# Optimization experiments

Measured on AMD Instinct MI355X. Metric: run time of the kernel, lower is better.

## Reference

```python
import jax, jax.numpy as jnp
import numpy as np

B = 4096
IN = 1024
H = 1024
S = 64   # num_memory_slots
Q = 16   # num_qubits_per_slot
OUT = 1024


def setup_inputs() -> dict:
    key = jax.random.key(0)
    ks = jax.random.split(key, 14)
    sd = lambda fan_in: 1.0 / np.sqrt(fan_in)
    return {
        "x_t": jax.random.normal(ks[0], (B, IN), jnp.float32),
        "h_prev": jax.random.normal(ks[1], (B, H), jnp.float32),
        # input_layer: Linear(IN+H, H)
        "W_in": jax.random.normal(ks[2], (IN + H, H), jnp.float32) * sd(IN + H),
        "b_in": jnp.zeros((H,), jnp.float32),
        # query_generator: Linear(H, H)
        "W_q": jax.random.normal(ks[3], (H, H), jnp.float32) * sd(H),
        "b_q": jnp.zeros((H,), jnp.float32),
        # memory_slot_selector: Linear(H, S)
        "W_sel": jax.random.normal(ks[4], (H, S), jnp.float32) * sd(H),
        "b_sel": jnp.zeros((S,), jnp.float32),
        # per-slot quantum memory params (surrogate classical simulation):
        # encode hidden -> qubit rotation angles, expectation <Z>=cos(angle), decode back
        "Wm_enc": jax.random.normal(ks[5], (S, H, Q), jnp.float32) * sd(H),
        "theta": jax.random.normal(ks[6], (S, Q), jnp.float32) * 0.1,
        "Wm_dec": jax.random.normal(ks[7], (S, Q, H), jnp.float32) * sd(Q),
        "b_m": jnp.zeros((H,), jnp.float32),
        # output_gate_and_transform: Linear(2H, H+OUT)
        "W_og": jax.random.normal(ks[8], (2 * H, H + OUT), jnp.float32) * sd(2 * H),
        "b_og": jnp.zeros((H + OUT,), jnp.float32),
    }


def reference(x_t, h_prev, W_in, b_in, W_q, b_q, W_sel, b_sel,
              Wm_enc, theta, Wm_dec, b_m, W_og, b_og):
    # combined input -> intermediate hidden
    combined = jnp.concatenate([x_t, h_prev], axis=1)           # (B, IN+H)
    h_int = jnp.tanh(combined @ W_in + b_in)                    # (B, H)
    # attention query -> slot logits -> top-1 slot per sample
    query = h_int @ W_q + b_q                                   # (B, H)
    logits = query @ W_sel + b_sel                              # (B, S)
    attn = jax.nn.softmax(logits, axis=1)
    idx = jnp.argmax(attn, axis=1)                              # (B,) int
    # batched gather-compute (replaces Python loop over batch)
    Wi = Wm_enc[idx]                                            # (B, H, Q)
    th = theta[idx]                                             # (B, Q)
    Wo = Wm_dec[idx]                                            # (B, Q, H)
    angles = jnp.einsum('bh,bhq->bq', h_int, Wi) + th           # (B, Q)
    expz = jnp.cos(angles)                                      # qubit <Z> expectations
    m_t = jnp.tanh(jnp.einsum('bq,bqh->bh', expz, Wo) + b_m)    # (B, H)
    # gated output + next hidden
    combined_out = jnp.concatenate([h_int, m_t], axis=1)        # (B, 2H)
    goh = combined_out @ W_og + b_og                            # (B, H+OUT)
    h_next = jnp.tanh(goh[:, :H])
    y_t = goh[:, H:]
    return (y_t, h_next)
```

## Files before the change

kernel.cpp:

```cpp
#include <hip/hip_runtime.h>
#include <math.h>


typedef __attribute__((ext_vector_type(4))) float floatx4;
typedef __attribute__((ext_vector_type(8))) _Float16 half8;
typedef __attribute__((ext_vector_type(4))) _Float16 half4;

#define OUT_H_OFF 4194304
#define TAU 8e-3f
#define FIX_CAP 512

#define AS1 __attribute__((address_space(1)))
#define AS3 __attribute__((address_space(3)))
#define GLL(gptr, lptr) __builtin_amdgcn_global_load_lds((const AS1 void*)(gptr), (AS3 void*)(lptr), 16, 0, 0)

__device__ __forceinline__ _Float16 f2h(float f) { return (_Float16)f; }

__global__ __launch_bounds__(256) void k_transpose(const float* __restrict__ W,
                                                   _Float16* __restrict__ BT) {
  __shared__ float tile[64][65];
  const int k0 = blockIdx.x * 64, n0 = blockIdx.y * 64;
  const int t = threadIdx.x, c = t & 63, rr = t >> 6;
#pragma unroll
  for (int i = 0; i < 16; ++i) {
    int r = i * 4 + rr;
    tile[r][c] = W[(size_t)(k0 + r) * 2048 + n0 + c];
  }
  __syncthreads();
#pragma unroll
  for (int i = 0; i < 16; ++i) {
    int r = i * 4 + rr;
    BT[(size_t)(n0 + r) * 2048 + k0 + c] = f2h(tile[c][r]);
  }
}

__global__ __launch_bounds__(256) void k_convA(const float* __restrict__ x_t, const float* __restrict__ h_prev,
                                               _Float16* __restrict__ A1) {
  const int stride = gridDim.x * blockDim.x;
  for (int c = blockIdx.x * blockDim.x + threadIdx.x; c < 2097152; c += stride) {
    int m = c >> 9, kc = (c & 511) << 2;
    const float* src = (kc < 1024) ? (x_t + (size_t)m * 1024 + kc)
                                   : (h_prev + (size_t)m * 1024 + (kc - 1024));
    floatx4 v = *reinterpret_cast<const floatx4*>(src);
    half4 h = {f2h(v[0]), f2h(v[1]), f2h(v[2]), f2h(v[3])};
    *reinterpret_cast<half4*>(&A1[(size_t)m * 2048 + kc]) = h;
  }
}

__global__ __launch_bounds__(256) void k_convB(const float* __restrict__ W_in,
                                               _Float16* __restrict__ BTin) {
  __shared__ float tile[64][65];
  const int k0 = blockIdx.x * 64, n0 = blockIdx.y * 64;
  const int t = threadIdx.x, c = t & 63, rr = t >> 6;
#pragma unroll
  for (int i = 0; i < 16; ++i) {
    int r = i * 4 + rr;
    tile[r][c] = W_in[(size_t)(k0 + r) * 1024 + n0 + c];
  }
  __syncthreads();
#pragma unroll
  for (int i = 0; i < 16; ++i) {
    int r = i * 4 + rr;
    BTin[(size_t)(n0 + r) * 2048 + k0 + c] = f2h(tile[c][r]);
  }
}

__global__ __launch_bounds__(256) void k_gemm1h(const _Float16* __restrict__ A1,
                                                const _Float16* __restrict__ BTin,
                                                const float* __restrict__ b_in,
                                                float* __restrict__ h_int, _Float16* __restrict__ A2) {
  __shared__ __align__(16) _Float16 As[4 * 4096];
  __shared__ __align__(16) _Float16 Bs[4 * 2048];
  const int t = threadIdx.x;
  const int lane = t & 63, w = t >> 6;
  const int wm = w >> 1, wn = w & 1;
  const int m0 = blockIdx.x * 128, n0 = blockIdx.y * 64;
  const int lr = lane & 15, lk = lane >> 4;
  floatx4 acc[4][2];
  floatx4 zero = {0.f, 0.f, 0.f, 0.f};
#pragma unroll
  for (int mi = 0; mi < 4; ++mi)
#pragma unroll
    for (int ni = 0; ni < 2; ++ni) acc[mi][ni] = zero;

  auto stage = [&](int p, int kt) {
    const int k0 = kt * 32;
#pragma unroll
    for (int j = 0; j < 2; ++j) {
      int cc = j * 256 + t;
      int row = cc >> 2, sl = cc & 3;
      int sg = sl ^ ((row >> 1) & 3);
      size_t ga = (size_t)(m0 + row) * 2048 + k0 + sg * 8;
      GLL(A1 + ga, &As[p * 4096 + cc * 8]);
    }
    {
      int cc = t;
      int row = cc >> 2, sl = cc & 3;
      int sg = sl ^ ((row >> 1) & 3);
      size_t gb = (size_t)(n0 + row) * 2048 + k0 + sg * 8;
      GLL(BTin + gb, &Bs[p * 2048 + cc * 8]);
    }
  };
  auto compute = [&](int p) {
    half8 af[4], bf[2];
#pragma unroll
    for (int mi = 0; mi < 4; ++mi) {
      int row = wm * 64 + mi * 16 + lr;
      int sl = lk ^ ((row >> 1) & 3);
      af[mi] = *reinterpret_cast<const half8*>(&As[p * 4096 + row * 32 + sl * 8]);
    }
#pragma unroll
    for (int ni = 0; ni < 2; ++ni) {
      int row = wn * 32 + ni * 16 + lr;
      int sl = lk ^ ((row >> 1) & 3);
      bf[ni] = *reinterpret_cast<const half8*>(&Bs[p * 2048 + row * 32 + sl * 8]);
    }
#pragma unroll
    for (int mi = 0; mi < 4; ++mi)
#pragma unroll
      for (int ni = 0; ni < 2; ++ni)
        acc[mi][ni] = __builtin_amdgcn_mfma_f32_16x16x32_f16(af[mi], bf[ni], acc[mi][ni], 0, 0, 0);
  };

  stage(0, 0);
  stage(1, 1);
  stage(2, 2);
  for (int kt = 0; kt < 64; ++kt) {
    __builtin_amdgcn_sched_barrier(0);
    if (kt < 62) {
      asm volatile("s_waitcnt vmcnt(6)" ::: "memory");
    } else if (kt == 62) {
      asm volatile("s_waitcnt vmcnt(3)" ::: "memory");
    } else {
      asm volatile("s_waitcnt vmcnt(0)" ::: "memory");
    }
    __builtin_amdgcn_s_barrier();
    __builtin_amdgcn_sched_barrier(0);
    if (kt + 3 < 64) stage((kt + 3) & 3, kt + 3);
    compute(kt & 3);
  }

#pragma unroll
  for (int mi = 0; mi < 4; ++mi) {
#pragma unroll
    for (int ni = 0; ni < 2; ++ni) {
      int gn = n0 + wn * 32 + ni * 16 + lr;
      float bias = b_in[gn];
      int gmb = m0 + wm * 64 + mi * 16 + lk * 4;
#pragma unroll
      for (int j = 0; j < 4; ++j) {
        int gm = gmb + j;
        float v = tanhf(acc[mi][ni][j] + bias);
        h_int[(size_t)gm * 1024 + gn] = v;
        A2[(size_t)gm * 2048 + gn] = f2h(v);
      }
    }
  }
}

__global__ __launch_bounds__(256) void k_gemm1(const float* __restrict__ x_t, const float* __restrict__ h_prev,
                                               const float* __restrict__ W_in, const float* __restrict__ b_in,
                                               float* __restrict__ h_int, _Float16* __restrict__ A2) {
  __shared__ float As[16 * 128];
  __shared__ float Bs[16 * 64];
  const int t = threadIdx.x;
  const int m0 = blockIdx.x * 128, n0 = blockIdx.y * 64;
  const int ty = t >> 4, tx = t & 15;
  float acc[8][4];
#pragma unroll
  for (int i = 0; i < 8; ++i)
#pragma unroll
    for (int j = 0; j < 4; ++j) acc[i][j] = 0.f;
  for (int kt = 0; kt < 128; ++kt) {
    const int k0 = kt * 16;
    __syncthreads();
#pragma unroll
    for (int u = 0; u < 2; ++u) {
      int cc = t + u * 256;
      int row = cc >> 2, col4 = (cc & 3) << 2;
      int gk = k0 + col4;
      const float* src = (gk < 1024) ? (x_t + (size_t)(m0 + row) * 1024 + gk)
                                     : (h_prev + (size_t)(m0 + row) * 1024 + (gk - 1024));
      floatx4 v = *reinterpret_cast<const floatx4*>(src);
      As[(col4 + 0) * 128 + row] = v[0];
      As[(col4 + 1) * 128 + row] = v[1];
      As[(col4 + 2) * 128 + row] = v[2];
      As[(col4 + 3) * 128 + row] = v[3];
    }
    {
      int kr = t >> 4, c4 = (t & 15) << 2;
      *reinterpret_cast<floatx4*>(&Bs[kr * 64 + c4]) =
          *reinterpret_cast<const floatx4*>(&W_in[(size_t)(k0 + kr) * 1024 + n0 + c4]);
    }
    __syncthreads();
#pragma unroll
    for (int kk = 0; kk < 16; ++kk) {
      floatx4 a0 = *reinterpret_cast<const floatx4*>(&As[kk * 128 + ty * 8]);
      floatx4 a1 = *reinterpret_cast<const floatx4*>(&As[kk * 128 + ty * 8 + 4]);
      floatx4 b = *reinterpret_cast<const floatx4*>(&Bs[kk * 64 + tx * 4]);
#pragma unroll
      for (int j = 0; j < 4; ++j) {
        acc[0][j] += a0[0] * b[j]; acc[1][j] += a0[1] * b[j];
        acc[2][j] += a0[2] * b[j]; acc[3][j] += a0[3] * b[j];
        acc[4][j] += a1[0] * b[j]; acc[5][j] += a1[1] * b[j];
        acc[6][j] += a1[2] * b[j]; acc[7][j] += a1[3] * b[j];
      }
    }
  }
  const int nbase = n0 + tx * 4;
  floatx4 bias = *reinterpret_cast<const floatx4*>(&b_in[nbase]);
#pragma unroll
  for (int i = 0; i < 8; ++i) {
    int gm = m0 + ty * 8 + i;
    floatx4 tv; half4 pk;
#pragma unroll
    for (int j = 0; j < 4; ++j) {
      float v = tanhf(acc[i][j] + bias[j]);
      tv[j] = v; pk[j] = f2h(v);
    }
    *reinterpret_cast<floatx4*>(&h_int[(size_t)gm * 1024 + nbase]) = tv;
    *reinterpret_cast<half4*>(&A2[(size_t)gm * 2048 + nbase]) = pk;
  }
}

__global__ __launch_bounds__(256) void k_wqs(const float* __restrict__ W_q, const float* __restrict__ b_q,
                                             const float* __restrict__ W_sel, const float* __restrict__ b_sel,
                                             float* __restrict__ Wqs) {
  const int t = threadIdx.x;
  const int w = t >> 6, lane = t & 63;
  const int h = blockIdx.x * 4 + w;
  if (h > 1024) return;
  const float* src = (h < 1024) ? (W_q + (size_t)h * 1024) : b_q;
  float acc = 0.f;
  for (int j = 0; j < 1024; j += 4) {
    floatx4 v = *reinterpret_cast<const floatx4*>(&src[j]);
    acc += v[0] * W_sel[(j + 0) * 64 + lane];
    acc += v[1] * W_sel[(j + 1) * 64 + lane];
    acc += v[2] * W_sel[(j + 2) * 64 + lane];
    acc += v[3] * W_sel[(j + 3) * 64 + lane];
  }
  if (h == 1024) acc += b_sel[lane];
  Wqs[(size_t)h * 64 + lane] = acc;
}

__global__ __launch_bounds__(256) void k_argmax(const float* __restrict__ h_int, const float* __restrict__ Wqs,
                                                int* __restrict__ idx, int* __restrict__ counter,
                                                int* __restrict__ list, float tau) {
  __shared__ float Ahs[64 * 32];
  __shared__ float Wt[64 * 64];
  const int t = threadIdx.x;
  const int r0 = blockIdx.x * 32;
  const int w = t >> 6, lane = t & 63;
  float acc[8];
#pragma unroll
  for (int i = 0; i < 8; ++i) acc[i] = 0.f;

  for (int kt = 0; kt < 16; ++kt) {
    const int k0 = kt * 64;
    __syncthreads();
#pragma unroll
    for (int u = 0; u < 2; ++u) {
      int cc = t + u * 256;
      int r = cc >> 4, k4 = (cc & 15) << 2;
      floatx4 v = *reinterpret_cast<const floatx4*>(&h_int[(size_t)(r0 + r) * 1024 + k0 + k4]);
      Ahs[(k4 + 0) * 32 + r] = v[0];
      Ahs[(k4 + 1) * 32 + r] = v[1];
      Ahs[(k4 + 2) * 32 + r] = v[2];
      Ahs[(k4 + 3) * 32 + r] = v[3];
    }
#pragma unroll
    for (int u = 0; u < 4; ++u) {
      int cc = t + u * 256;
      int kr = cc >> 4, c4 = (cc & 15) << 2;
      *reinterpret_cast<floatx4*>(&Wt[kr * 64 + c4]) =
          *reinterpret_cast<const floatx4*>(&Wqs[(size_t)(k0 + kr) * 64 + c4]);
    }
    __syncthreads();
#pragma unroll
    for (int k = 0; k < 64; ++k) {
      float wv = Wt[k * 64 + lane];
      floatx4 a0 = *reinterpret_cast<const floatx4*>(&Ahs[k * 32 + w * 8]);
      floatx4 a1 = *reinterpret_cast<const floatx4*>(&Ahs[k * 32 + w * 8 + 4]);
      acc[0] += a0[0] * wv; acc[1] += a0[1] * wv; acc[2] += a0[2] * wv; acc[3] += a0[3] * wv;
      acc[4] += a1[0] * wv; acc[5] += a1[1] * wv; acc[6] += a1[2] * wv; acc[7] += a1[3] * wv;
    }
  }
  const float bqs = Wqs[1024 * 64 + lane];
#pragma unroll
  for (int i = 0; i < 8; ++i) {
    float v1 = acc[i] + bqs;
    int i1 = lane;
    float v2 = -__builtin_inff();
#pragma unroll
    for (int off = 32; off >= 1; off >>= 1) {
      float ov1 = __shfl_xor(v1, off);
      int oi1 = __shfl_xor(i1, off);
      float ov2 = __shfl_xor(v2, off);
      if (ov1 > v1 || (ov1 == v1 && oi1 < i1)) {
        v2 = fmaxf(v1, ov2); v1 = ov1; i1 = oi1;
      } else {
        v2 = fmaxf(v2, ov1);
      }
    }
    if (lane == 0) {
      int row = r0 + w * 8 + i;
      idx[row] = i1;
      if (v1 - v2 < tau) {
        int pos = atomicAdd(counter, 1);
        if (pos < FIX_CAP) list[pos] = row;
      }
    }
  }
}

__global__ __launch_bounds__(256) void k_fixA(const float* __restrict__ x_t, const float* __restrict__ h_prev,
                                              const float* __restrict__ W_in, const int* __restrict__ counter,
                                              const int* __restrict__ list, float* __restrict__ scratch) {
  __shared__ float cmb[256];
  const int t = threadIdx.x;
  const int cnt = min(counter[0], FIX_CAP);
  const int nwork = cnt * 8;
  for (int e = blockIdx.x; e < nwork; e += gridDim.x) {
    const int r = list[e >> 3], kc = e & 7;
    __syncthreads();
    {
      int k = kc * 256 + t;
      cmb[t] = (k < 1024) ? x_t[(size_t)r * 1024 + k] : h_prev[(size_t)r * 1024 + (k - 1024)];
    }
    __syncthreads();
    floatx4 a = {0.f, 0.f, 0.f, 0.f};
    const int n4 = t * 4;
    const float* Wb = W_in + (size_t)(kc * 256) * 1024 + n4;
    for (int kk = 0; kk < 256; ++kk) {
      float c = cmb[kk];
      floatx4 wv = *reinterpret_cast<const floatx4*>(Wb + (size_t)kk * 1024);
      a[0] += c * wv[0]; a[1] += c * wv[1]; a[2] += c * wv[2]; a[3] += c * wv[3];
    }
    *reinterpret_cast<floatx4*>(&scratch[(size_t)e * 1024 + n4]) = a;
  }
}

__global__ __launch_bounds__(256) void k_fixB(const float* __restrict__ scratch, const float* __restrict__ b_in,
                                              const float* __restrict__ Wqs, const int* __restrict__ counter,
                                              const int* __restrict__ list, int* __restrict__ idx) {
  __shared__ float hrow[1024];
  __shared__ float partial[4 * 64];
  __shared__ float lg[64];
  const int t = threadIdx.x;
  const int cnt = min(counter[0], FIX_CAP);
  const int e = blockIdx.x;
  if (e >= cnt) return;
  const int r = list[e];
  const int n4 = t * 4;
  floatx4 a = *reinterpret_cast<const floatx4*>(&b_in[n4]);
#pragma unroll
  for (int kc = 0; kc < 8; ++kc) {
    floatx4 p = *reinterpret_cast<const floatx4*>(&scratch[(size_t)(e * 8 + kc) * 1024 + n4]);
    a[0] += p[0]; a[1] += p[1]; a[2] += p[2]; a[3] += p[3];
  }
  hrow[n4 + 0] = tanhf(a[0]);
  hrow[n4 + 1] = tanhf(a[1]);
  hrow[n4 + 2] = tanhf(a[2]);
  hrow[n4 + 3] = tanhf(a[3]);
  __syncthreads();
  const int s = t & 63, part = t >> 6;
  const int hb0 = part * 256;
  const float* Wp = Wqs + (size_t)hb0 * 64 + s;
  float p0 = 0.f, p1 = 0.f, p2 = 0.f, p3 = 0.f, p4 = 0.f, p5 = 0.f, p6 = 0.f, p7 = 0.f;
  for (int h8 = 0; h8 < 256; h8 += 8) {
    float w0 = Wp[(size_t)(h8 + 0) * 64];
    float w1 = Wp[(size_t)(h8 + 1) * 64];
    float w2 = Wp[(size_t)(h8 + 2) * 64];
    float w3 = Wp[(size_t)(h8 + 3) * 64];
    float w4 = Wp[(size_t)(h8 + 4) * 64];
    float w5 = Wp[(size_t)(h8 + 5) * 64];
    float w6 = Wp[(size_t)(h8 + 6) * 64];
    float w7 = Wp[(size_t)(h8 + 7) * 64];
    const int hb = hb0 + h8;
    p0 += hrow[hb + 0] * w0;
    p1 += hrow[hb + 1] * w1;
    p2 += hrow[hb + 2] * w2;
    p3 += hrow[hb + 3] * w3;
    p4 += hrow[hb + 4] * w4;
    p5 += hrow[hb + 5] * w5;
    p6 += hrow[hb + 6] * w6;
    p7 += hrow[hb + 7] * w7;
  }
  partial[part * 64 + s] = ((p0 + p1) + (p2 + p3)) + ((p4 + p5) + (p6 + p7));
  __syncthreads();
  if (t < 64) lg[t] = partial[t] + partial[64 + t] + partial[128 + t] + partial[192 + t] + Wqs[1024 * 64 + t];
  __syncthreads();
  if (t == 0) {
    float bv = lg[0]; int bi = 0;
    for (int ss = 1; ss < 64; ++ss) {
      if (lg[ss] > bv) { bv = lg[ss]; bi = ss; }
    }
    idx[r] = bi;
  }
}

__global__ __launch_bounds__(256) void k_mix(const float* __restrict__ h_int, const int* __restrict__ idx,
                                             const float* __restrict__ Wm_enc, const float* __restrict__ theta,
                                             const float* __restrict__ Wm_dec, const float* __restrict__ b_m,
                                             _Float16* __restrict__ A2) {
  __shared__ float hrow[1024];
  __shared__ float partial[256];
  __shared__ float expz[16];
  const int b = blockIdx.x, t = threadIdx.x;
  const int s = idx[b];
  *reinterpret_cast<floatx4*>(&hrow[t * 4]) =
      *reinterpret_cast<const floatx4*>(&h_int[(size_t)b * 1024 + t * 4]);
  __syncthreads();
  const int q = t & 15, g = t >> 4;
  const float* We = Wm_enc + (size_t)s * 16384;
  float p = 0.f;
#pragma unroll 8
  for (int j = 0; j < 64; ++j) {
    int h = g + j * 16;
    p += hrow[h] * We[h * 16 + q];
  }
  partial[t] = p;
  __syncthreads();
  if (t < 16) {
    float a = 0.f;
#pragma unroll
    for (int g2 = 0; g2 < 16; ++g2) a += partial[g2 * 16 + t];
    a += theta[s * 16 + t];
    expz[t] = cosf(a);
  }
  __syncthreads();
  const float* Wd = Wm_dec + (size_t)s * 16384;
  float e[16];
#pragma unroll
  for (int qq = 0; qq < 16; ++qq) e[qq] = expz[qq];
#pragma unroll
  for (int r = 0; r < 4; ++r) {
    int h = r * 256 + t;
    float v = b_m[h];
#pragma unroll
    for (int qq = 0; qq < 16; ++qq) v += e[qq] * Wd[qq * 1024 + h];
    A2[(size_t)b * 2048 + 1024 + h] = f2h(tanhf(v));
  }
}

__global__ __launch_bounds__(256) void k_gemm4h(const _Float16* __restrict__ A2,
                                                const _Float16* __restrict__ BT,
                                                const float* __restrict__ b_og, float* __restrict__ out) {
  __shared__ __align__(16) _Float16 As[4 * 4096];
  __shared__ __align__(16) _Float16 Bs[4 * 4096];
  const int t = threadIdx.x;
  const int lane = t & 63, w = t >> 6;
  const int wm = w >> 1, wn = w & 1;
  const int m0 = blockIdx.x * 128, n0 = blockIdx.y * 128;
  const int lr = lane & 15, lk = lane >> 4;
  floatx4 acc[4][4];
  floatx4 zero = {0.f, 0.f, 0.f, 0.f};
#pragma unroll
  for (int mi = 0; mi < 4; ++mi)
#pragma unroll
    for (int ni = 0; ni < 4; ++ni) acc[mi][ni] = zero;

  auto stage = [&](int p, int kt) {
    const int k0 = kt * 32;
#pragma unroll
    for (int j = 0; j < 2; ++j) {
      int cc = j * 256 + t;
      int row = cc >> 2, sl = cc & 3;
      int sg = sl ^ ((row >> 1) & 3);
      size_t ga = (size_t)(m0 + row) * 2048 + k0 + sg * 8;
      size_t gb = (size_t)(n0 + row) * 2048 + k0 + sg * 8;
      GLL(A2 + ga, &As[p * 4096 + cc * 8]);
      GLL(BT + gb, &Bs[p * 4096 + cc * 8]);
    }
  };
  auto compute = [&](int p) {
    half8 af[4], bf[4];
#pragma unroll
    for (int mi = 0; mi < 4; ++mi) {
      int row = wm * 64 + mi * 16 + lr;
      int sl = lk ^ ((row >> 1) & 3);
      af[mi] = *reinterpret_cast<const half8*>(&As[p * 4096 + row * 32 + sl * 8]);
    }
#pragma unroll
    for (int ni = 0; ni < 4; ++ni) {
      int row = wn * 64 + ni * 16 + lr;
      int sl = lk ^ ((row >> 1) & 3);
      bf[ni] = *reinterpret_cast<const half8*>(&Bs[p * 4096 + row * 32 + sl * 8]);
    }
#pragma unroll
    for (int mi = 0; mi < 4; ++mi)
#pragma unroll
      for (int ni = 0; ni < 4; ++ni)
        acc[mi][ni] = __builtin_amdgcn_mfma_f32_16x16x32_f16(af[mi], bf[ni], acc[mi][ni], 0, 0, 0);
  };

  stage(0, 0);
  stage(1, 1);
  stage(2, 2);
  for (int kt = 0; kt < 64; ++kt) {
    __builtin_amdgcn_sched_barrier(0);
    if (kt < 62) {
      asm volatile("s_waitcnt vmcnt(8)" ::: "memory");
    } else if (kt == 62) {
      asm volatile("s_waitcnt vmcnt(4)" ::: "memory");
    } else {
      asm volatile("s_waitcnt vmcnt(0)" ::: "memory");
    }
    __builtin_amdgcn_s_barrier();
    __builtin_amdgcn_sched_barrier(0);
    if (kt + 3 < 64) stage((kt + 3) & 3, kt + 3);
    compute(kt & 3);
  }

#pragma unroll
  for (int mi = 0; mi < 4; ++mi) {
#pragma unroll
    for (int ni = 0; ni < 4; ++ni) {
      int gn = n0 + wn * 64 + ni * 16 + lr;
      float bias = b_og[gn];
      int gmb = m0 + wm * 64 + mi * 16 + lk * 4;
#pragma unroll
      for (int j = 0; j < 4; ++j) {
        int gm = gmb + j;
        float v = acc[mi][ni][j] + bias;
        if (gn < 1024) {
          out[OUT_H_OFF + (size_t)gm * 1024 + gn] = tanhf(v);
        } else {
          out[(size_t)gm * 1024 + (gn - 1024)] = v;
        }
      }
    }
  }
}

extern "C" void kernel_launch(void* const* d_in, const int* in_sizes, int n_in,
                              void* d_out, int out_size, void* d_ws, size_t ws_size,
                              hipStream_t stream) {
  (void)in_sizes; (void)n_in; (void)out_size;
  const float* x_t    = (const float*)d_in[0];
  const float* h_prev = (const float*)d_in[1];
  const float* W_in   = (const float*)d_in[2];
  const float* b_in   = (const float*)d_in[3];
  const float* W_q    = (const float*)d_in[4];
  const float* b_q    = (const float*)d_in[5];
  const float* W_sel  = (const float*)d_in[6];
  const float* b_sel  = (const float*)d_in[7];
  const float* Wm_enc = (const float*)d_in[8];
  const float* theta  = (const float*)d_in[9];
  const float* Wm_dec = (const float*)d_in[10];
  const float* b_m    = (const float*)d_in[11];
  const float* W_og   = (const float*)d_in[12];
  const float* b_og   = (const float*)d_in[13];
  float* out = (float*)d_out;

  char* ws = (char*)d_ws;
  float* h_int          = (float*)(ws);
  _Float16* A2          = (_Float16*)(ws + ((size_t)16 << 20));
  _Float16* BT          = (_Float16*)(ws + ((size_t)32 << 20));
  float* Wqs            = (float*)(ws + ((size_t)40 << 20));
  int* idx              = (int*)(ws + ((size_t)41 << 20));
  int* counter          = (int*)(ws + ((size_t)41 << 20) + 16384);
  int* list             = (int*)(ws + ((size_t)41 << 20) + 16384 + 64);
  _Float16* A1          = (_Float16*)(ws + ((size_t)42 << 20));
  _Float16* BTin        = (_Float16*)(ws + ((size_t)58 << 20));
  float* fix_scratch    = (float*)(ws + ((size_t)62 << 20));

  const bool use_mfma = ws_size >= ((size_t)82 << 20);

  hipLaunchKernelGGL(k_transpose, dim3(32, 32), dim3(256), 0, stream, W_og, BT);
  hipLaunchKernelGGL(k_wqs, dim3(257), dim3(256), 0, stream, W_q, b_q, W_sel, b_sel, Wqs);
  hipMemsetAsync(counter, 0, 4, stream);

  if (use_mfma) {
    hipLaunchKernelGGL(k_convA, dim3(2048), dim3(256), 0, stream, x_t, h_prev, A1);
    hipLaunchKernelGGL(k_convB, dim3(32, 16), dim3(256), 0, stream, W_in, BTin);
    hipLaunchKernelGGL(k_gemm1h, dim3(32, 16), dim3(256), 0, stream,
                       A1, BTin, b_in, h_int, A2);
    hipLaunchKernelGGL(k_argmax, dim3(128), dim3(256), 0, stream, h_int, Wqs, idx, counter, list, TAU);
    hipLaunchKernelGGL(k_fixA, dim3(512), dim3(256), 0, stream,
                       x_t, h_prev, W_in, counter, list, fix_scratch);
    hipLaunchKernelGGL(k_fixB, dim3(FIX_CAP), dim3(256), 0, stream,
                       fix_scratch, b_in, Wqs, counter, list, idx);
  } else {
    hipLaunchKernelGGL(k_gemm1, dim3(32, 16), dim3(256), 0, stream, x_t, h_prev, W_in, b_in, h_int, A2);
    hipLaunchKernelGGL(k_argmax, dim3(128), dim3(256), 0, stream, h_int, Wqs, idx, counter, list, 0.0f);
  }

  hipLaunchKernelGGL(k_mix, dim3(4096), dim3(256), 0, stream, h_int, idx, Wm_enc, theta, Wm_dec, b_m, A2);
  hipLaunchKernelGGL(k_gemm4h, dim3(32, 16), dim3(256), 0, stream, A2, BT, b_og, out);
}
```

Baseline: 282.8 us.

## Batch fp32 fix-up GEMM over rows to reuse W_in loads

Rewrites the fp32 recompute kernel for near-tie rows. It now tiles 8 listed rows against 64 output columns per block and accumulates over the full K inside each block. Before, each work item streamed the whole W_in K-chunk for a single row and wrote 8 partial sums per row. Each W_in element loaded is now reused across 8 rows, and the partial-sum reduction in k_fixB is removed. The risk is lower parallelism when the fix list is small.

```diff
diff --git a/kernel.cpp b/kernel.cpp
--- a/kernel.cpp
+++ b/kernel.cpp
@@ -313,30 +313,55 @@
   }
 }
 
-__global__ __launch_bounds__(256) void k_fixA(const float* __restrict__ x_t, const float* __restrict__ h_prev,
-                                              const float* __restrict__ W_in, const int* __restrict__ counter,
-                                              const int* __restrict__ list, float* __restrict__ scratch) {
-  __shared__ float cmb[256];
+__global__ __launch_bounds__(256) void k_fixA2(const float* __restrict__ x_t, const float* __restrict__ h_prev,
+                                               const float* __restrict__ W_in, const int* __restrict__ counter,
+                                               const int* __restrict__ list, float* __restrict__ scratch) {
+  __shared__ float xr[8][260];
   const int t = threadIdx.x;
   const int cnt = min(counter[0], FIX_CAP);
-  const int nwork = cnt * 8;
-  for (int e = blockIdx.x; e < nwork; e += gridDim.x) {
-    const int r = list[e >> 3], kc = e & 7;
+  const int nbatch = (cnt + 7) >> 3;
+  const int col = blockIdx.x * 64 + (t & 63);
+  const int rp = t >> 6;
+  for (int mb = blockIdx.y; mb < nbatch; mb += gridDim.y) {
+    const int rbase = mb * 8;
+    float a0[4] = {0.f, 0.f, 0.f, 0.f};
+    float a1[4] = {0.f, 0.f, 0.f, 0.f};
+    for (int kc = 0; kc < 8; ++kc) {
+      __syncthreads();
+      {
+        int r = t >> 5;
+        int kl = (t & 31) * 8;
+        int e = rbase + r;
+        int row = list[e < cnt ? e : 0];
+        int kg = kc * 256 + kl;
+        const float* src = (kg < 1024) ? (x_t + (size_t)row * 1024 + kg)
+                                       : (h_prev + (size_t)row * 1024 + (kg - 1024));
+        floatx4 v0 = *reinterpret_cast<const floatx4*>(src);
+        floatx4 v1 = *reinterpret_cast<const floatx4*>(src + 4);
+        *reinterpret_cast<floatx4*>(&xr[r][kl]) = v0;
+        *reinterpret_cast<floatx4*>(&xr[r][kl + 4]) = v1;
+      }
+      __syncthreads();
+      const float* Wb = W_in + (size_t)(kc * 256) * 1024 + col;
+      const float* x0 = xr[rp * 2];
+      const float* x1 = xr[rp * 2 + 1];
+      for (int kk = 0; kk < 256; kk += 4) {
+        float w0 = Wb[(size_t)(kk + 0) * 1024];
+        float w1 = Wb[(size_t)(kk + 1) * 1024];
+        float w2 = Wb[(size_t)(kk + 2) * 1024];
+        float w3 = Wb[(size_t)(kk + 3) * 1024];
+        a0[0] += x0[kk + 0] * w0; a1[0] += x1[kk + 0] * w0;
+        a0[1] += x0[kk + 1] * w1; a1[1] += x1[kk + 1] * w1;
+        a0[2] += x0[kk + 2] * w2; a1[2] += x1[kk + 2] * w2;
+        a0[3] += x0[kk + 3] * w3; a1[3] += x1[kk + 3] * w3;
+      }
+    }
+    float z0 = (a0[0] + a0[1]) + (a0[2] + a0[3]);
+    float z1 = (a1[0] + a1[1]) + (a1[2] + a1[3]);
+    int e0 = rbase + rp * 2, e1 = e0 + 1;
+    if (e0 < cnt) scratch[(size_t)e0 * 1024 + col] = z0;
+    if (e1 < cnt) scratch[(size_t)e1 * 1024 + col] = z1;
     __syncthreads();
-    {
-      int k = kc * 256 + t;
-      cmb[t] = (k < 1024) ? x_t[(size_t)r * 1024 + k] : h_prev[(size_t)r * 1024 + (k - 1024)];
-    }
-    __syncthreads();
-    floatx4 a = {0.f, 0.f, 0.f, 0.f};
-    const int n4 = t * 4;
-    const float* Wb = W_in + (size_t)(kc * 256) * 1024 + n4;
-    for (int kk = 0; kk < 256; ++kk) {
-      float c = cmb[kk];
-      floatx4 wv = *reinterpret_cast<const floatx4*>(Wb + (size_t)kk * 1024);
-      a[0] += c * wv[0]; a[1] += c * wv[1]; a[2] += c * wv[2]; a[3] += c * wv[3];
-    }
-    *reinterpret_cast<floatx4*>(&scratch[(size_t)e * 1024 + n4]) = a;
   }
 }
 
@@ -352,16 +377,12 @@
   if (e >= cnt) return;
   const int r = list[e];
   const int n4 = t * 4;
-  floatx4 a = *reinterpret_cast<const floatx4*>(&b_in[n4]);
-#pragma unroll
-  for (int kc = 0; kc < 8; ++kc) {
-    floatx4 p = *reinterpret_cast<const floatx4*>(&scratch[(size_t)(e * 8 + kc) * 1024 + n4]);
-    a[0] += p[0]; a[1] += p[1]; a[2] += p[2]; a[3] += p[3];
-  }
-  hrow[n4 + 0] = tanhf(a[0]);
-  hrow[n4 + 1] = tanhf(a[1]);
-  hrow[n4 + 2] = tanhf(a[2]);
-  hrow[n4 + 3] = tanhf(a[3]);
+  floatx4 b4 = *reinterpret_cast<const floatx4*>(&b_in[n4]);
+  floatx4 z4 = *reinterpret_cast<const floatx4*>(&scratch[(size_t)e * 1024 + n4]);
+  hrow[n4 + 0] = tanhf(z4[0] + b4[0]);
+  hrow[n4 + 1] = tanhf(z4[1] + b4[1]);
+  hrow[n4 + 2] = tanhf(z4[2] + b4[2]);
+  hrow[n4 + 3] = tanhf(z4[3] + b4[3]);
   __syncthreads();
   const int s = t & 63, part = t >> 6;
   const int hb0 = part * 256;
@@ -577,7 +598,7 @@
     hipLaunchKernelGGL(k_gemm1h, dim3(32, 16), dim3(256), 0, stream,
                        A1, BTin, b_in, h_int, A2);
     hipLaunchKernelGGL(k_argmax, dim3(128), dim3(256), 0, stream, h_int, Wqs, idx, counter, list, TAU);
-    hipLaunchKernelGGL(k_fixA, dim3(512), dim3(256), 0, stream,
+    hipLaunchKernelGGL(k_fixA2, dim3(16, 64), dim3(256), 0, stream,
                        x_t, h_prev, W_in, counter, list, fix_scratch);
     hipLaunchKernelGGL(k_fixB, dim3(FIX_CAP), dim3(256), 0, stream,
                        fix_scratch, b_in, Wqs, counter, list, idx);
```

New measurement: 302.6 us. 1.07x slower.
